# Kernel tuning notes

Hardware: AMD Instinct MI355X
Metric: run time of the kernel (lower is better)

Reference implementation:

```python
import jax, jax.numpy as jnp
import numpy as np
import math

B, T, D = 2, 2048, 1024
H, DH = 16, 64          # num_heads, head_dim
DFF = 4096              # 4*d_model
EPS = 1e-5


def _layernorm(x, g, b):
    m = jnp.mean(x, axis=-1, keepdims=True)
    v = jnp.mean(jnp.square(x - m), axis=-1, keepdims=True)
    return (x - m) * jax.lax.rsqrt(v + EPS) * g + b


def setup_inputs() -> dict:
    key = jax.random.key(0)
    ks = jax.random.split(key, 6)
    s = 0.02
    return {
        "x": jax.random.normal(ks[0], (B, T, D), dtype=jnp.float32),
        "ln1_g": jnp.ones((D,), jnp.float32), "ln1_b": jnp.zeros((D,), jnp.float32),
        "ln2_g": jnp.ones((D,), jnp.float32), "ln2_b": jnp.zeros((D,), jnp.float32),
        "w_qkv": jax.random.normal(ks[1], (3 * D, D), jnp.float32) * s,
        "b_qkv": jnp.zeros((3 * D,), jnp.float32),
        "w_out": jax.random.normal(ks[2], (D, D), jnp.float32) * s,
        "b_out": jnp.zeros((D,), jnp.float32),
        "w1": jax.random.normal(ks[3], (DFF, D), jnp.float32) * s,
        "b1": jnp.zeros((DFF,), jnp.float32),
        "w2": jax.random.normal(ks[4], (D, DFF), jnp.float32) * s,
        "b2": jnp.zeros((D,), jnp.float32),
    }


def reference(x, ln1_g, ln1_b, ln2_g, ln2_b, w_qkv, b_qkv, w_out, b_out, w1, b1, w2, b2):
    # --- attention sublayer (Pre-LN) ---
    h = _layernorm(x, ln1_g, ln1_b)                       # [B,T,D]
    qkv = h @ w_qkv.T + b_qkv                             # [B,T,3D]
    qkv = qkv.reshape(B, T, 3, H, DH).transpose(2, 0, 3, 1, 4)  # [3,B,H,T,DH]
    q, k, v = qkv[0], qkv[1], qkv[2]
    scores = jnp.einsum('bhqd,bhkd->bhqk', q, k) / math.sqrt(DH)  # [B,H,T,T]
    causal = jnp.tril(jnp.ones((T, T), dtype=bool))
    scores = jnp.where(causal, scores, -jnp.inf)
    weights = jax.nn.softmax(scores, axis=-1)
    attn = jnp.einsum('bhqk,bhkd->bhqd', weights, v)      # [B,H,T,DH]
    attn = attn.transpose(0, 2, 1, 3).reshape(B, T, D)
    x = x + (attn @ w_out.T + b_out)

    # --- FFN sublayer (Pre-LN, exact GELU) ---
    h2 = _layernorm(x, ln2_g, ln2_b)
    ff = jax.nn.gelu(h2 @ w1.T + b1, approximate=False) @ w2.T + b2
    return x + ff
```

## Files before the change

kernel.cpp:

```cpp
#include <hip/hip_runtime.h>
#include <hip/hip_bf16.h>
#include <cmath>

typedef __bf16 bf16x8 __attribute__((ext_vector_type(8)));
typedef float  f32x4  __attribute__((ext_vector_type(4)));

#define LDS_AS __attribute__((address_space(3)))
#define GLB_AS __attribute__((address_space(1)))

__device__ __forceinline__ void gll16(const void* g, void* l) {
    __builtin_amdgcn_global_load_lds((const GLB_AS unsigned int*)g,
                                     (LDS_AS unsigned int*)l, 16, 0, 0);
}

__device__ __forceinline__ f32x4 mfma16(bf16x8 a, bf16x8 b, f32x4 c) {
    return __builtin_amdgcn_mfma_f32_16x16x32_bf16(a, b, c, 0, 0, 0);
}

__device__ __forceinline__ unsigned short f2bf(float f) {
    __hip_bfloat16 b = __float2bfloat16(f);
    return *reinterpret_cast<unsigned short*>(&b);
}

__device__ __forceinline__ bf16x8 swzfrag(const __hip_bfloat16* __restrict__ lds,
                                          int row, int cb)
{
    const int addr = row * 128 + (cb ^ ((row & 7) << 4));
    return *(const bf16x8*)((const char*)lds + addr);
}

__device__ __forceinline__ void stage64x128B(const char* __restrict__ base, int pitch,
                                             char* __restrict__ lds, int t)
{
#pragma unroll
    for (int i = 0; i < 2; ++i) {
        const int d   = i * 4096 + t * 16;
        const int row = d >> 7;
        const int x   = d & 127;
        const int gx  = x ^ ((row & 7) << 4);
        gll16(base + (size_t)row * pitch + gx, lds + d);
    }
}

__device__ __forceinline__ void stage128x128B(const char* __restrict__ base, int pitch,
                                              char* __restrict__ lds, int t)
{
#pragma unroll
    for (int i = 0; i < 4; ++i) {
        const int d   = i * 4096 + t * 16;
        const int row = d >> 7;
        const int x   = d & 127;
        const int gx  = x ^ ((row & 7) << 4);
        gll16(base + (size_t)row * pitch + gx, lds + d);
    }
}

#define TB   2
#define TT   2048
#define TD   1024
#define TH   16
#define TDH  64
#define TDFF 4096
#define TM   4096

__global__ __launch_bounds__(256)
void cvt_kernel(const float* __restrict__ src, __hip_bfloat16* __restrict__ dst, int n4)
{
    int i = blockIdx.x * 256 + threadIdx.x;
    if (i >= n4) return;
    float4 v = ((const float4*)src)[i];
    ushort4 o;
    o.x = f2bf(v.x); o.y = f2bf(v.y); o.z = f2bf(v.z); o.w = f2bf(v.w);
    ((ushort4*)dst)[i] = o;
}

__global__ __launch_bounds__(256)
void ln_kernel(const float* __restrict__ x, const float* __restrict__ g,
               const float* __restrict__ b, __hip_bfloat16* __restrict__ out)
{
    const int row = blockIdx.x;
    const int t = threadIdx.x;
    const float4 v = *(const float4*)(x + (size_t)row * TD + t * 4);
    float s  = v.x + v.y + v.z + v.w;
    float ss = v.x*v.x + v.y*v.y + v.z*v.z + v.w*v.w;
#pragma unroll
    for (int d = 1; d < 64; d <<= 1) { s += __shfl_xor(s, d); ss += __shfl_xor(ss, d); }
    __shared__ float red[8];
    const int wv = t >> 6, lane = t & 63;
    if (lane == 0) { red[wv] = s; red[4 + wv] = ss; }
    __syncthreads();
    s  = red[0] + red[1] + red[2] + red[3];
    ss = red[4] + red[5] + red[6] + red[7];
    const float mean = s * (1.0f / TD);
    const float var  = ss * (1.0f / TD) - mean * mean;
    const float rstd = rsqrtf(var + 1e-5f);
    const float4 gv = *(const float4*)(g + t * 4);
    const float4 bv = *(const float4*)(b + t * 4);
    ushort4 o;
    o.x = f2bf((v.x - mean) * rstd * gv.x + bv.x);
    o.y = f2bf((v.y - mean) * rstd * gv.y + bv.y);
    o.z = f2bf((v.z - mean) * rstd * gv.z + bv.z);
    o.w = f2bf((v.w - mean) * rstd * gv.w + bv.w);
    *(ushort4*)(out + (size_t)row * TD + t * 4) = o;
}

template<int EPI>
__global__ __launch_bounds__(256)
void gemm_bt(const __hip_bfloat16* __restrict__ A, const __hip_bfloat16* __restrict__ Bw,
             const float* __restrict__ bias, const float* __restrict__ resid,
             float* __restrict__ outf, __hip_bfloat16* __restrict__ outb,
             __hip_bfloat16* __restrict__ qb, __hip_bfloat16* __restrict__ kb,
             __hip_bfloat16* __restrict__ vtb,
             int M, int N, int K)
{
    __shared__ __hip_bfloat16 ldsA[2][128 * 64];
    __shared__ __hip_bfloat16 ldsB[2][128 * 64];
    const int t = threadIdx.x;
    const int lane = t & 63, wv = t >> 6;
    const int wr = wv >> 1, wc = wv & 1;
    const int l15 = lane & 15, lg = lane >> 4;

    const int nbn = gridDim.x;
    const int L   = blockIdx.y * nbn + blockIdx.x;
    const int cpx = (nbn * gridDim.y) >> 3;
    const int swz = (L & 7) * cpx + (L >> 3);
    const int bm  = swz / nbn;
    const int bn  = swz - bm * nbn;

    f32x4 acc[4][4] = {};

    const char* Ab = (const char*)(A  + (size_t)bm * 128 * K);
    const char* Bb = (const char*)(Bw + (size_t)bn * 128 * K);
    const int pitch = K * 2;

    const int nt = K >> 6;
    stage128x128B(Ab, pitch, (char*)ldsA[0], t);
    stage128x128B(Bb, pitch, (char*)ldsB[0], t);

    int cur = 0;
    for (int it = 0; it < nt; ++it) {
        if (it + 1 < nt) {
            const size_t koff = (size_t)(it + 1) * 128;
            stage128x128B(Ab + koff, pitch, (char*)ldsA[cur ^ 1], t);
            stage128x128B(Bb + koff, pitch, (char*)ldsB[cur ^ 1], t);
            asm volatile("s_waitcnt vmcnt(8)" ::: "memory");
        } else {
            asm volatile("s_waitcnt vmcnt(0)" ::: "memory");
        }
        __builtin_amdgcn_s_barrier();
        __builtin_amdgcn_sched_barrier(0);
        bf16x8 af[4][2], bfr[4][2];
#pragma unroll
        for (int mf = 0; mf < 4; ++mf)
#pragma unroll
            for (int kk = 0; kk < 2; ++kk)
                af[mf][kk] = swzfrag(ldsA[cur], wr * 64 + mf * 16 + l15, kk * 64 + lg * 16);
#pragma unroll
        for (int nf = 0; nf < 4; ++nf)
#pragma unroll
            for (int kk = 0; kk < 2; ++kk)
                bfr[nf][kk] = swzfrag(ldsB[cur], wc * 64 + nf * 16 + l15, kk * 64 + lg * 16);
        __builtin_amdgcn_s_setprio(1);
#pragma unroll
        for (int mf = 0; mf < 4; ++mf)
#pragma unroll
            for (int nf = 0; nf < 4; ++nf) {
                acc[mf][nf] = mfma16(af[mf][0], bfr[nf][0], acc[mf][nf]);
                acc[mf][nf] = mfma16(af[mf][1], bfr[nf][1], acc[mf][nf]);
            }
        __builtin_amdgcn_s_setprio(0);
        __builtin_amdgcn_s_barrier();
        cur ^= 1;
    }

#pragma unroll
    for (int mf = 0; mf < 4; ++mf) {
#pragma unroll
        for (int nf = 0; nf < 4; ++nf) {
#pragma unroll
            for (int r = 0; r < 4; ++r) {
                const int mg = bm * 128 + wr * 64 + mf * 16 + lg * 4 + r;
                const int ng = bn * 128 + wc * 64 + nf * 16 + l15;
                float v = acc[mf][nf][r] + bias[ng];
                if constexpr (EPI == 1) {
                    const size_t o = (size_t)mg * N + ng;
                    outf[o] = v + resid[o];
                } else if constexpr (EPI == 2) {
                    const float ge = 0.5f * v * (1.0f + erff(v * 0.70710678118654752f));
                    outb[(size_t)mg * N + ng] = __float2bfloat16(ge);
                } else {
                    const int which = ng >> 10;
                    const int hh = (ng >> 6) & 15;
                    const int dh = ng & 63;
                    const int bb = mg >> 11;
                    const int tt = mg & 2047;
                    const int bhid = bb * TH + hh;
                    const __hip_bfloat16 bv = __float2bfloat16(v);
                    if (which == 0)      qb[((size_t)bhid * TT + tt) * TDH + dh] = bv;
                    else if (which == 1) kb[((size_t)bhid * TT + tt) * TDH + dh] = bv;
                    else                 vtb[((size_t)bhid * TDH + dh) * TT + tt] = bv;
                }
            }
        }
    }
}

__global__ __launch_bounds__(256)
void flash_kernel(const __hip_bfloat16* __restrict__ q, const __hip_bfloat16* __restrict__ k,
                  const __hip_bfloat16* __restrict__ vt, __hip_bfloat16* __restrict__ attn)
{
    const int L  = blockIdx.y * gridDim.x + blockIdx.x;
    const int cu = L & 255;
    const int s  = L >> 8;
    const int q0 = cu & 31;
    const int qt = (s & 1) ? (31 - q0) : q0;
    const int bh = s * 8 + (cu >> 5);

    const int t = threadIdx.x;
    const int w = t >> 6, lane = t & 63;
    const int l15 = lane & 15, lg = lane >> 4;
    const int qrow0 = qt * 64 + w * 16;
    const __hip_bfloat16* Qb = q  + (size_t)bh * TT * TDH;
    const __hip_bfloat16* Kb = k  + (size_t)bh * TT * TDH;
    const __hip_bfloat16* Vb = vt + (size_t)bh * TDH * TT;

    __shared__ __hip_bfloat16 kt[2][64 * 64];
    __shared__ __hip_bfloat16 vtt[2][64 * 64];
    __shared__ __hip_bfloat16 plds[4][16 * 64];

    bf16x8 qa[2];
#pragma unroll
    for (int c = 0; c < 2; ++c)
        qa[c] = *(const bf16x8*)(Qb + (size_t)(qrow0 + l15) * TDH + c * 32 + lg * 8);

    f32x4 o[4] = {};
    float mrun = -INFINITY, lrun = 0.0f;

    const int nt = qt + 1;
    int cur = 0;
    stage64x128B((const char*)Kb, 128, (char*)kt[0], t);
    stage64x128B((const char*)Vb, TT * 2, (char*)vtt[0], t);
    __syncthreads();

    for (int it = 0; it < nt; ++it) {
        const int kv0 = it * 64;
        if (it + 1 < nt) {
            stage64x128B((const char*)Kb + (size_t)(kv0 + 64) * 128, 128, (char*)kt[cur ^ 1], t);
            stage64x128B((const char*)Vb + (size_t)(kv0 + 64) * 2, TT * 2, (char*)vtt[cur ^ 1], t);
        }
        f32x4 sc[4] = {};
#pragma unroll
        for (int j = 0; j < 4; ++j) {
            const bf16x8 kb0 = swzfrag(kt[cur], j * 16 + l15, lg * 16);
            const bf16x8 kb1 = swzfrag(kt[cur], j * 16 + l15, 64 + lg * 16);
            sc[j] = mfma16(kb0, qa[0], sc[j]);
            sc[j] = mfma16(kb1, qa[1], sc[j]);
        }
        if (it == nt - 1) {
            const int qg = qrow0 + l15;
#pragma unroll
            for (int j = 0; j < 4; ++j)
#pragma unroll
                for (int r = 0; r < 4; ++r) {
                    const int kvg = kv0 + j * 16 + lg * 4 + r;
                    sc[j][r] = (kvg <= qg) ? sc[j][r] * 0.125f : -INFINITY;
                }
        } else {
#pragma unroll
            for (int j = 0; j < 4; ++j)
#pragma unroll
                for (int r = 0; r < 4; ++r) sc[j][r] *= 0.125f;
        }
        float pm;
        {
            float m0 = fmaxf(fmaxf(sc[0][0], sc[0][1]), fmaxf(sc[0][2], sc[0][3]));
            float m1 = fmaxf(fmaxf(sc[1][0], sc[1][1]), fmaxf(sc[1][2], sc[1][3]));
            float m2 = fmaxf(fmaxf(sc[2][0], sc[2][1]), fmaxf(sc[2][2], sc[2][3]));
            float m3 = fmaxf(fmaxf(sc[3][0], sc[3][1]), fmaxf(sc[3][2], sc[3][3]));
            pm = fmaxf(fmaxf(m0, m1), fmaxf(m2, m3));
        }
        pm = fmaxf(pm, __shfl_xor(pm, 16));
        pm = fmaxf(pm, __shfl_xor(pm, 32));

        const float mn = fmaxf(mrun, pm);
        const float alpha = __expf(mrun - mn);
        mrun = mn;
        f32x4 p[4];
        float rs = 0.0f;
#pragma unroll
        for (int j = 0; j < 4; ++j) {
            float a = 0.0f;
#pragma unroll
            for (int r = 0; r < 4; ++r) { p[j][r] = __expf(sc[j][r] - mn); a += p[j][r]; }
            rs += a;
        }
        rs += __shfl_xor(rs, 16);
        rs += __shfl_xor(rs, 32);
        lrun = lrun * alpha + rs;
#pragma unroll
        for (int nf = 0; nf < 4; ++nf)
#pragma unroll
            for (int r = 0; r < 4; ++r) o[nf][r] *= alpha;
        {
            __hip_bfloat16* pw = plds[w];
#pragma unroll
            for (int j = 0; j < 4; ++j) {
                ushort4 pk;
                pk.x = f2bf(p[j][0]); pk.y = f2bf(p[j][1]);
                pk.z = f2bf(p[j][2]); pk.w = f2bf(p[j][3]);
                const int cb = j * 32 + lg * 8;
                *(ushort4*)((char*)pw + l15 * 128 + (cb ^ ((l15 & 7) << 4))) = pk;
            }
        }
        asm volatile("s_waitcnt lgkmcnt(0)" ::: "memory");
        __builtin_amdgcn_sched_barrier(0);
        bf16x8 pb[2];
#pragma unroll
        for (int c = 0; c < 2; ++c)
            pb[c] = swzfrag(plds[w], l15, c * 64 + lg * 16);
#pragma unroll
        for (int nf = 0; nf < 4; ++nf) {
            const bf16x8 vb0 = swzfrag(vtt[cur], nf * 16 + l15, lg * 16);
            const bf16x8 vb1 = swzfrag(vtt[cur], nf * 16 + l15, 64 + lg * 16);
            o[nf] = mfma16(vb0, pb[0], o[nf]);
            o[nf] = mfma16(vb1, pb[1], o[nf]);
        }
        __syncthreads();
        cur ^= 1;
    }

    const int bb = bh >> 4, hh = bh & 15;
    const float inv = 1.0f / lrun;
    const int tt = qrow0 + l15;
#pragma unroll
    for (int nf = 0; nf < 4; ++nf) {
        const int d0 = nf * 16 + lg * 4;
        ushort4 st;
        st.x = f2bf(o[nf][0] * inv);
        st.y = f2bf(o[nf][1] * inv);
        st.z = f2bf(o[nf][2] * inv);
        st.w = f2bf(o[nf][3] * inv);
        *(ushort4*)(attn + ((size_t)(bb * TT + tt)) * TD + hh * TDH + d0) = st;
    }
}

extern "C" void kernel_launch(void* const* d_in, const int* in_sizes, int n_in,
                              void* d_out, int out_size, void* d_ws, size_t ws_size,
                              hipStream_t stream)
{
    const float* x     = (const float*)d_in[0];
    const float* ln1_g = (const float*)d_in[1];
    const float* ln1_b = (const float*)d_in[2];
    const float* ln2_g = (const float*)d_in[3];
    const float* ln2_b = (const float*)d_in[4];
    const float* w_qkv = (const float*)d_in[5];
    const float* b_qkv = (const float*)d_in[6];
    const float* w_out = (const float*)d_in[7];
    const float* b_out = (const float*)d_in[8];
    const float* w1    = (const float*)d_in[9];
    const float* b1    = (const float*)d_in[10];
    const float* w2    = (const float*)d_in[11];
    const float* b2    = (const float*)d_in[12];

    char* ws = (char*)d_ws;
    __hip_bfloat16* wqkv_bf = (__hip_bfloat16*)(ws + 0);
    __hip_bfloat16* wout_bf = (__hip_bfloat16*)(ws + 6291456);
    __hip_bfloat16* w1_bf   = (__hip_bfloat16*)(ws + 8388608);
    __hip_bfloat16* w2_bf   = (__hip_bfloat16*)(ws + 16777216);
    float*          x2      = (float*)(ws + 25165824);
    __hip_bfloat16* hbuf    = (__hip_bfloat16*)(ws + 41943040);
    __hip_bfloat16* qbuf    = (__hip_bfloat16*)(ws + 50331648);
    __hip_bfloat16* kbuf    = (__hip_bfloat16*)(ws + 58720256);
    __hip_bfloat16* vtbuf   = (__hip_bfloat16*)(ws + 67108864);
    __hip_bfloat16* attnbuf = (__hip_bfloat16*)(ws + 75497472);
    __hip_bfloat16* ff1     = (__hip_bfloat16*)(ws + 50331648);

    cvt_kernel<<<3072, 256, 0, stream>>>(w_qkv, wqkv_bf, 3 * TD * TD / 4);
    cvt_kernel<<<1024, 256, 0, stream>>>(w_out, wout_bf, TD * TD / 4);
    cvt_kernel<<<4096, 256, 0, stream>>>(w1, w1_bf, TDFF * TD / 4);
    cvt_kernel<<<4096, 256, 0, stream>>>(w2, w2_bf, TD * TDFF / 4);

    ln_kernel<<<TM, 256, 0, stream>>>(x, ln1_g, ln1_b, hbuf);
    gemm_bt<0><<<dim3(24, 32), 256, 0, stream>>>(hbuf, wqkv_bf, b_qkv, nullptr,
                                                 nullptr, nullptr, qbuf, kbuf, vtbuf,
                                                 TM, 3 * TD, TD);
    flash_kernel<<<dim3(32, 32), 256, 0, stream>>>(qbuf, kbuf, vtbuf, attnbuf);
    gemm_bt<1><<<dim3(8, 32), 256, 0, stream>>>(attnbuf, wout_bf, b_out, x,
                                                x2, nullptr, nullptr, nullptr, nullptr,
                                                TM, TD, TD);
    ln_kernel<<<TM, 256, 0, stream>>>(x2, ln2_g, ln2_b, hbuf);
    gemm_bt<2><<<dim3(32, 32), 256, 0, stream>>>(hbuf, w1_bf, b1, nullptr,
                                                 nullptr, ff1, nullptr, nullptr, nullptr,
                                                 TM, TDFF, TD);
    gemm_bt<1><<<dim3(8, 32), 256, 0, stream>>>(ff1, w2_bf, b2, x2,
                                                (float*)d_out, nullptr, nullptr, nullptr, nullptr,
                                                TM, TD, TDFF);
}
```

Before: 281.4 us.

## Deepen GEMM pipeline to four-stage ring with 32-wide K tiles

Result: slower. 315.3 us (+12.1%).

```diff
diff --git a/kernel.cpp b/kernel.cpp
--- a/kernel.cpp
+++ b/kernel.cpp
@@ -42,15 +42,22 @@
     }
 }
 
-__device__ __forceinline__ void stage128x128B(const char* __restrict__ base, int pitch,
-                                              char* __restrict__ lds, int t)
-{
-#pragma unroll
-    for (int i = 0; i < 4; ++i) {
+__device__ __forceinline__ bf16x8 swzfrag32(const __hip_bfloat16* __restrict__ lds,
+                                            int row, int cb)
+{
+    const int addr = row * 64 + (cb ^ ((row & 3) << 4));
+    return *(const bf16x8*)((const char*)lds + addr);
+}
+
+__device__ __forceinline__ void stage128x64B(const char* __restrict__ base, int pitch,
+                                             char* __restrict__ lds, int t)
+{
+#pragma unroll
+    for (int i = 0; i < 2; ++i) {
         const int d   = i * 4096 + t * 16;
-        const int row = d >> 7;
-        const int x   = d & 127;
-        const int gx  = x ^ ((row & 7) << 4);
+        const int row = d >> 6;
+        const int x   = d & 63;
+        const int gx  = x ^ ((row & 3) << 4);
         gll16(base + (size_t)row * pitch + gx, lds + d);
     }
 }
@@ -113,8 +120,8 @@
              __hip_bfloat16* __restrict__ vtb,
              int M, int N, int K)
 {
-    __shared__ __hip_bfloat16 ldsA[2][128 * 64];
-    __shared__ __hip_bfloat16 ldsB[2][128 * 64];
+    __shared__ __hip_bfloat16 ldsA[4][128 * 32];
+    __shared__ __hip_bfloat16 ldsB[4][128 * 32];
     const int t = threadIdx.x;
     const int lane = t & 63, wv = t >> 6;
     const int wr = wv >> 1, wc = wv & 1;
@@ -133,44 +140,46 @@
     const char* Bb = (const char*)(Bw + (size_t)bn * 128 * K);
     const int pitch = K * 2;
 
-    const int nt = K >> 6;
-    stage128x128B(Ab, pitch, (char*)ldsA[0], t);
-    stage128x128B(Bb, pitch, (char*)ldsB[0], t);
-
-    int cur = 0;
+    const int nt = K >> 5;
+    stage128x64B(Ab,       pitch, (char*)ldsA[0], t);
+    stage128x64B(Bb,       pitch, (char*)ldsB[0], t);
+    stage128x64B(Ab + 64,  pitch, (char*)ldsA[1], t);
+    stage128x64B(Bb + 64,  pitch, (char*)ldsB[1], t);
+    stage128x64B(Ab + 128, pitch, (char*)ldsA[2], t);
+    stage128x64B(Bb + 128, pitch, (char*)ldsB[2], t);
+
     for (int it = 0; it < nt; ++it) {
-        if (it + 1 < nt) {
-            const size_t koff = (size_t)(it + 1) * 128;
-            stage128x128B(Ab + koff, pitch, (char*)ldsA[cur ^ 1], t);
-            stage128x128B(Bb + koff, pitch, (char*)ldsB[cur ^ 1], t);
+        if (it + 3 < nt) {
+            const size_t koff = (size_t)(it + 3) * 64;
+            stage128x64B(Ab + koff, pitch, (char*)ldsA[(it + 3) & 3], t);
+            stage128x64B(Bb + koff, pitch, (char*)ldsB[(it + 3) & 3], t);
+            asm volatile("s_waitcnt vmcnt(12)" ::: "memory");
+        } else if (it + 2 < nt) {
             asm volatile("s_waitcnt vmcnt(8)" ::: "memory");
+        } else if (it + 1 < nt) {
+            asm volatile("s_waitcnt vmcnt(4)" ::: "memory");
         } else {
             asm volatile("s_waitcnt vmcnt(0)" ::: "memory");
         }
         __builtin_amdgcn_s_barrier();
         __builtin_amdgcn_sched_barrier(0);
-        bf16x8 af[4][2], bfr[4][2];
+        const __hip_bfloat16* bufA = ldsA[it & 3];
+        const __hip_bfloat16* bufB = ldsB[it & 3];
+        bf16x8 af[4], bfr[4];
 #pragma unroll
         for (int mf = 0; mf < 4; ++mf)
-#pragma unroll
-            for (int kk = 0; kk < 2; ++kk)
-                af[mf][kk] = swzfrag(ldsA[cur], wr * 64 + mf * 16 + l15, kk * 64 + lg * 16);
+            af[mf] = swzfrag32(bufA, wr * 64 + mf * 16 + l15, lg * 16);
 #pragma unroll
         for (int nf = 0; nf < 4; ++nf)
-#pragma unroll
-            for (int kk = 0; kk < 2; ++kk)
-                bfr[nf][kk] = swzfrag(ldsB[cur], wc * 64 + nf * 16 + l15, kk * 64 + lg * 16);
+            bfr[nf] = swzfrag32(bufB, wc * 64 + nf * 16 + l15, lg * 16);
         __builtin_amdgcn_s_setprio(1);
 #pragma unroll
         for (int mf = 0; mf < 4; ++mf)
 #pragma unroll
-            for (int nf = 0; nf < 4; ++nf) {
-                acc[mf][nf] = mfma16(af[mf][0], bfr[nf][0], acc[mf][nf]);
-                acc[mf][nf] = mfma16(af[mf][1], bfr[nf][1], acc[mf][nf]);
-            }
+            for (int nf = 0; nf < 4; ++nf)
+                acc[mf][nf] = mfma16(af[mf], bfr[nf], acc[mf][nf]);
         __builtin_amdgcn_s_setprio(0);
         __builtin_amdgcn_s_barrier();
-        cur ^= 1;
     }
 
 #pragma unroll
```
